# Optimization experiments

Hardware: AMD Instinct MI355X
Metric: run time of the kernel (lower is better)

Reference implementation:

```python
import jax, jax.numpy as jnp
import numpy as np

D_MODEL = 768
D_STATE = 16
D_CONV = 4
EXPAND = 2
HEADDIM = 64
D_INNER = EXPAND * D_MODEL          # 1536
NHEADS = D_INNER // HEADDIM         # 24
CONV_DIM = D_INNER + 2 * D_STATE    # 1568
D_IN_PROJ = 2 * D_INNER + 2 * D_STATE + NHEADS  # 3128
BATCH, SEQ = 4, 2048


def _mamba_params(key, scale=0.02):
    ks = jax.random.split(key, 5)
    return dict(
        in_w=jax.random.normal(ks[0], (D_MODEL, D_IN_PROJ), jnp.float32) * scale,
        conv_w=jax.random.normal(ks[1], (CONV_DIM, D_CONV), jnp.float32) * scale,
        conv_b=jnp.zeros((CONV_DIM,), jnp.float32),
        dt_bias=jax.random.normal(ks[2], (NHEADS,), jnp.float32) * 0.1,
        A_log=jnp.log(jax.random.uniform(ks[3], (NHEADS,), jnp.float32, 1.0, 16.0)),
        D=jnp.ones((NHEADS,), jnp.float32),
        norm_w=jnp.ones((D_INNER,), jnp.float32),
        out_w=jax.random.normal(ks[4], (D_INNER, D_MODEL), jnp.float32) * scale,
    )


def setup_inputs() -> dict:
    key = jax.random.key(0)
    kx, kf, kb, k1, k2 = jax.random.split(key, 5)
    f = _mamba_params(kf)
    b = _mamba_params(kb)
    k1a, k1b = jax.random.split(k1)
    inp = {
        'x': jax.random.normal(kx, (BATCH, SEQ, D_MODEL), jnp.float32),
        'ln1_w': jnp.ones((D_MODEL,), jnp.float32), 'ln1_b': jnp.zeros((D_MODEL,), jnp.float32),
        'ln2_w': jnp.ones((D_MODEL,), jnp.float32), 'ln2_b': jnp.zeros((D_MODEL,), jnp.float32),
        'ffn_w1': jax.random.normal(k1a, (2 * D_MODEL, 4 * D_MODEL), jnp.float32) * 0.02,
        'ffn_b1': jnp.zeros((4 * D_MODEL,), jnp.float32),
        'ffn_w2': jax.random.normal(k1b, (4 * D_MODEL, D_MODEL), jnp.float32) * 0.02,
        'ffn_b2': jnp.zeros((D_MODEL,), jnp.float32),
    }
    for name, p in (('f', f), ('b', b)):
        for k, v in p.items():
            inp[name + '_' + k] = v
    return inp


def _layernorm(x, w, b, eps=1e-5):
    m = jnp.mean(x, -1, keepdims=True)
    v = jnp.mean((x - m) ** 2, -1, keepdims=True)
    return (x - m) * jax.lax.rsqrt(v + eps) * w + b


def _mamba2(u, in_w, conv_w, conv_b, dt_bias, A_log, D, norm_w, out_w):
    b, l, _ = u.shape
    zxbcdt = u @ in_w                               # (b,l,d_in_proj)
    z = zxbcdt[..., :D_INNER]
    xBC = zxbcdt[..., D_INNER:D_INNER + CONV_DIM]
    dt = jax.nn.softplus(zxbcdt[..., -NHEADS:] + dt_bias)   # (b,l,h)
    # depthwise causal conv1d (kernel D_CONV) + SiLU
    xpad = jnp.pad(xBC, ((0, 0), (D_CONV - 1, 0), (0, 0)))
    xc = sum(conv_w[:, k] * xpad[:, k:k + l, :] for k in range(D_CONV)) + conv_b
    xc = jax.nn.silu(xc)
    xh = xc[..., :D_INNER].reshape(b, l, NHEADS, HEADDIM)
    Bm = xc[..., D_INNER:D_INNER + D_STATE]          # (b,l,n), ngroups=1
    Cm = xc[..., D_INNER + D_STATE:]                 # (b,l,n)
    A = -jnp.exp(A_log)                              # (h,)
    dA = jnp.exp(dt * A)                             # (b,l,h)

    def step(h, inp):
        dA_t, dt_t, B_t, C_t, x_t = inp              # (b,h),(b,h),(b,n),(b,n),(b,h,p)
        h = h * dA_t[:, :, None, None] + (dt_t[:, :, None] * x_t)[..., None] * B_t[:, None, None, :]
        y = jnp.einsum('bhpn,bn->bhp', h, C_t)
        return h, y

    h0 = jnp.zeros((b, NHEADS, HEADDIM, D_STATE), u.dtype)
    xs = (dA.transpose(1, 0, 2), dt.transpose(1, 0, 2), Bm.transpose(1, 0, 2),
          Cm.transpose(1, 0, 2), xh.transpose(1, 0, 2, 3))
    _, ys = jax.lax.scan(step, h0, xs)               # ys: (l,b,h,p)
    y = ys.transpose(1, 0, 2, 3) + D[None, None, :, None] * xh
    y = y.reshape(b, l, D_INNER)
    # gated RMSNorm: rmsnorm(y * silu(z)) * weight
    yz = y * jax.nn.silu(z)
    yz = yz * jax.lax.rsqrt(jnp.mean(yz * yz, -1, keepdims=True) + 1e-5) * norm_w
    return yz @ out_w


def reference(x, ln1_w, ln1_b, ln2_w, ln2_b,
              f_in_w, f_conv_w, f_conv_b, f_dt_bias, f_A_log, f_D, f_norm_w, f_out_w,
              b_in_w, b_conv_w, b_conv_b, b_dt_bias, b_A_log, b_D, b_norm_w, b_out_w,
              ffn_w1, ffn_b1, ffn_w2, ffn_b2):
    xn = _layernorm(x, ln1_w, ln1_b)
    fo = _mamba2(xn, f_in_w, f_conv_w, f_conv_b, f_dt_bias, f_A_log, f_D, f_norm_w, f_out_w)
    bo = _mamba2(jnp.flip(xn, 1), b_in_w, b_conv_w, b_conv_b, b_dt_bias, b_A_log, b_D, b_norm_w, b_out_w)
    bo = jnp.flip(bo, 1)
    bi = jnp.concatenate([fo, bo], -1)
    h = jax.nn.gelu(bi @ ffn_w1 + ffn_b1, approximate=False)
    h = jax.nn.gelu(h @ ffn_w2 + ffn_b2, approximate=False)
    # dropout is identity in eval mode
    return _layernorm(x + h, ln2_w, ln2_b)
```

## Files before the change

### kernel.cpp

```cpp
#include <hip/hip_runtime.h>
#include <math.h>

#define BATCH   4
#define SEQ     2048
#define DMODEL  768
#define DSTATE  16
#define DCONV   4
#define HEADDIM 64
#define DINNER  1536
#define NHEADS  24
#define CONVDIM 1568
#define DINPROJ 3128
#define DFFN    3072
#define ROWS    (BATCH*SEQ)
#define QCH     128
#define NCHUNK  (SEQ/QCH)

typedef __attribute__((ext_vector_type(8))) short bhalf8;
typedef __attribute__((ext_vector_type(4))) float floatx4;

__device__ __forceinline__ float gelu_f(float x) {
    return 0.5f * x * (1.0f + erff(x * 0.70710678118654752f));
}

__device__ __forceinline__ void splitRNE(float v, unsigned short& h, unsigned short& l) {
    unsigned u = __float_as_uint(v);
    unsigned rr = u + 0x7FFFu + ((u >> 16) & 1u);
    unsigned short hi = (unsigned short)(rr >> 16);
    float rem = v - __uint_as_float(((unsigned)hi) << 16);
    unsigned u2 = __float_as_uint(rem);
    unsigned r2 = u2 + 0x7FFFu + ((u2 >> 16) & 1u);
    h = hi;
    l = (unsigned short)(r2 >> 16);
}

__device__ __forceinline__ void gl16(const unsigned short* g, unsigned short* l) {
    __builtin_amdgcn_global_load_lds(
        (const __attribute__((address_space(1))) void*)g,
        (__attribute__((address_space(3))) void*)l, 16, 0, 0);
}

__device__ __forceinline__ float2 blockReduce2(float a, float b) {
    #pragma unroll
    for (int o = 32; o > 0; o >>= 1) {
        a += __shfl_down(a, o, 64);
        b += __shfl_down(b, o, 64);
    }
    __shared__ float sa[4], sb[4];
    int w = threadIdx.x >> 6, lane = threadIdx.x & 63;
    if (lane == 0) { sa[w] = a; sb[w] = b; }
    __syncthreads();
    if (threadIdx.x == 0) {
        int nw = blockDim.x >> 6;
        for (int i = 1; i < nw; ++i) { a += sa[i]; b += sb[i]; }
        sa[0] = a; sb[0] = b;
    }
    __syncthreads();
    return make_float2(sa[0], sb[0]);
}

__global__ __launch_bounds__(256) void ln_kernel(
    const float* __restrict__ x, const float* __restrict__ res,
    const float* __restrict__ w, const float* __restrict__ b,
    float* __restrict__ out)
{
    int r = blockIdx.x;
    const float* xr = x + (size_t)r * DMODEL;
    float v[3]; float s = 0.f, ss = 0.f;
    #pragma unroll
    for (int i = 0; i < 3; ++i) {
        int c = threadIdx.x + i * 256;
        float t = xr[c];
        if (res) t += res[(size_t)r * DMODEL + c];
        v[i] = t; s += t; ss += t * t;
    }
    float2 red = blockReduce2(s, ss);
    float mean = red.x * (1.0f / DMODEL);
    float var  = red.y * (1.0f / DMODEL) - mean * mean;
    float inv  = rsqrtf(var + 1e-5f);
    #pragma unroll
    for (int i = 0; i < 3; ++i) {
        int c = threadIdx.x + i * 256;
        out[(size_t)r * DMODEL + c] = (v[i] - mean) * inv * w[c] + b[c];
    }
}

__global__ __launch_bounds__(256) void ln_split_kernel(
    const float* __restrict__ x,
    const float* __restrict__ w, const float* __restrict__ b,
    unsigned short* __restrict__ H, unsigned short* __restrict__ L)
{
    int r = blockIdx.x;
    const float* xr = x + (size_t)r * DMODEL;
    float v[3]; float s = 0.f, ss = 0.f;
    #pragma unroll
    for (int i = 0; i < 3; ++i) {
        int c = threadIdx.x + i * 256;
        float t = xr[c];
        v[i] = t; s += t; ss += t * t;
    }
    float2 red = blockReduce2(s, ss);
    float mean = red.x * (1.0f / DMODEL);
    float var  = red.y * (1.0f / DMODEL) - mean * mean;
    float inv  = rsqrtf(var + 1e-5f);
    #pragma unroll
    for (int i = 0; i < 3; ++i) {
        int c = threadIdx.x + i * 256;
        float o = (v[i] - mean) * inv * w[c] + b[c];
        unsigned short h, l;
        splitRNE(o, h, l);
        H[(size_t)r * DMODEL + c] = h;
        L[(size_t)r * DMODEL + c] = l;
    }
}

__global__ __launch_bounds__(256) void wconv(
    const float* __restrict__ W, unsigned short* __restrict__ TH,
    unsigned short* __restrict__ TL, int K, int N)
{
    __shared__ float t[32][33];
    int tx = threadIdx.x & 31, ty = threadIdx.x >> 5;
    int kb = blockIdx.y * 32, nb = blockIdx.x * 32;
    #pragma unroll
    for (int i = 0; i < 4; ++i) {
        int k = kb + ty + i * 8, n = nb + tx;
        t[ty + i * 8][tx] = (k < K && n < N) ? W[(size_t)k * N + n] : 0.f;
    }
    __syncthreads();
    #pragma unroll
    for (int i = 0; i < 4; ++i) {
        int n = nb + ty + i * 8, k = kb + tx;
        if (n < N && k < K) {
            unsigned short hi, lo;
            splitRNE(t[tx][ty + i * 8], hi, lo);
            TH[(size_t)n * K + k] = hi;
            TL[(size_t)n * K + k] = lo;
        }
    }
}

__global__ __launch_bounds__(256) void gemm3(
    const unsigned short* __restrict__ AHg, const unsigned short* __restrict__ ALg,
    const unsigned short* __restrict__ BHg, const unsigned short* __restrict__ BLg,
    float* __restrict__ C, unsigned short* __restrict__ CHo, unsigned short* __restrict__ CLo,
    const float* __restrict__ bias,
    int M, int N, int K, int ldc, int coloff,
    int revA, int revC, int act)
{
    (void)M;
    __shared__ __align__(16) unsigned short AsH[128 * 32], AsL[128 * 32];
    __shared__ __align__(16) unsigned short BsH[128 * 32], BsL[128 * 32];

    const int tid = threadIdx.x;
    const int m0 = blockIdx.y * 128;
    const int n0 = blockIdx.x * 128;

    size_t aoff[2], boff[2];
    int lofs[2];
    #pragma unroll
    for (int q = 0; q < 2; ++q) {
        int row = (tid >> 2) + 64 * q;
        int sd  = (tid & 3) ^ ((row >> 1) & 3);
        int ar = m0 + row;
        if (revA) ar = (ar & ~(SEQ - 1)) + (SEQ - 1 - (ar & (SEQ - 1)));
        aoff[q] = (size_t)ar * K + sd * 8;
        boff[q] = (size_t)(n0 + row) * K + sd * 8;
        lofs[q] = (tid + 256 * q) * 8;
    }

    auto stage = [&](int k0) {
        #pragma unroll
        for (int q = 0; q < 2; ++q) {
            gl16(AHg + aoff[q] + k0, AsH + lofs[q]);
            gl16(ALg + aoff[q] + k0, AsL + lofs[q]);
            gl16(BHg + boff[q] + k0, BsH + lofs[q]);
            gl16(BLg + boff[q] + k0, BsL + lofs[q]);
        }
    };

    auto frag = [&](const unsigned short* buf, int row, int slot) -> bhalf8 {
        int sp = slot ^ ((row >> 1) & 3);
        return *(const bhalf8*)(buf + row * 32 + sp * 8);
    };

    const int w = tid >> 6, lane = tid & 63;
    const int rw = (w >> 1) * 64, cw = (w & 1) * 64;
    const int lr = lane & 15;
    const int lq = lane >> 4;

    floatx4 acc[4][4];
    const floatx4 fz = {0.f, 0.f, 0.f, 0.f};
    #pragma unroll
    for (int i = 0; i < 4; ++i)
        #pragma unroll
        for (int j = 0; j < 4; ++j) acc[i][j] = fz;

    const int ktiles = K >> 5;
    stage(0);
    for (int kt = 0; kt < ktiles; ++kt) {
        __syncthreads();
        bhalf8 ah[4], al[4], bh[4], bl[4];
        #pragma unroll
        for (int i = 0; i < 4; ++i) {
            int ra = rw + i * 16 + lr;
            int rb = cw + i * 16 + lr;
            ah[i] = frag(AsH, ra, lq);
            al[i] = frag(AsL, ra, lq);
            bh[i] = frag(BsH, rb, lq);
            bl[i] = frag(BsL, rb, lq);
        }
        __syncthreads();
        if (kt + 1 < ktiles) stage((kt + 1) * 32);
        #pragma unroll
        for (int i = 0; i < 4; ++i)
            #pragma unroll
            for (int j = 0; j < 4; ++j) {
                acc[i][j] = __builtin_amdgcn_mfma_f32_16x16x32_bf16(ah[i], bh[j], acc[i][j], 0, 0, 0);
                acc[i][j] = __builtin_amdgcn_mfma_f32_16x16x32_bf16(ah[i], bl[j], acc[i][j], 0, 0, 0);
                acc[i][j] = __builtin_amdgcn_mfma_f32_16x16x32_bf16(al[i], bh[j], acc[i][j], 0, 0, 0);
            }
    }

    #pragma unroll
    for (int i = 0; i < 4; ++i) {
        #pragma unroll
        for (int j = 0; j < 4; ++j) {
            int gc = n0 + cw + j * 16 + lr;
            if (gc < N) {
                float bv = bias ? bias[gc] : 0.f;
                #pragma unroll
                for (int rg = 0; rg < 4; ++rg) {
                    int gm = m0 + rw + i * 16 + lq * 4 + rg;
                    if (revC) gm = (gm & ~(SEQ - 1)) + (SEQ - 1 - (gm & (SEQ - 1)));
                    float v = acc[i][j][rg] + bv;
                    if (act) v = gelu_f(v);
                    size_t o = (size_t)gm * ldc + coloff + gc;
                    if (CHo) {
                        unsigned short h, l;
                        splitRNE(v, h, l);
                        CHo[o] = h; CLo[o] = l;
                    } else {
                        C[o] = v;
                    }
                }
            }
        }
    }
}

__global__ __launch_bounds__(64) void gemm1w(
    const unsigned short* __restrict__ AHg, const unsigned short* __restrict__ ALg,
    const unsigned short* __restrict__ BHg, const unsigned short* __restrict__ BLg,
    float* __restrict__ C, unsigned short* __restrict__ CHo, unsigned short* __restrict__ CLo,
    const float* __restrict__ bias,
    int M, int N, int K, int ldc, int coloff,
    int revA, int revC, int act)
{
    (void)M;
    __shared__ __align__(16) unsigned short AsH[64 * 32], AsL[64 * 32];
    __shared__ __align__(16) unsigned short BsH[64 * 32], BsL[64 * 32];

    const int tid = threadIdx.x;
    const int m0 = blockIdx.y * 64;
    const int n0 = blockIdx.x * 64;

    size_t aoff[4], boff[4];
    int lofs[4];
    #pragma unroll
    for (int q = 0; q < 4; ++q) {
        int row = (tid >> 2) + 16 * q;
        int sd  = (tid & 3) ^ ((row >> 1) & 3);
        int ar = m0 + row;
        if (revA) ar = (ar & ~(SEQ - 1)) + (SEQ - 1 - (ar & (SEQ - 1)));
        aoff[q] = (size_t)ar * K + sd * 8;
        boff[q] = (size_t)(n0 + row) * K + sd * 8;
        lofs[q] = (tid + 64 * q) * 8;
    }

    auto stage = [&](int k0) {
        #pragma unroll
        for (int q = 0; q < 4; ++q) {
            gl16(AHg + aoff[q] + k0, AsH + lofs[q]);
            gl16(ALg + aoff[q] + k0, AsL + lofs[q]);
            gl16(BHg + boff[q] + k0, BsH + lofs[q]);
            gl16(BLg + boff[q] + k0, BsL + lofs[q]);
        }
    };

    auto frag = [&](const unsigned short* buf, int row, int slot) -> bhalf8 {
        int sp = slot ^ ((row >> 1) & 3);
        return *(const bhalf8*)(buf + row * 32 + sp * 8);
    };

    const int lr = tid & 15;
    const int lq = tid >> 4;

    floatx4 acc[4][4];
    const floatx4 fz = {0.f, 0.f, 0.f, 0.f};
    #pragma unroll
    for (int i = 0; i < 4; ++i)
        #pragma unroll
        for (int j = 0; j < 4; ++j) acc[i][j] = fz;

    const int ktiles = K >> 5;
    stage(0);
    for (int kt = 0; kt < ktiles; ++kt) {
        asm volatile("s_waitcnt vmcnt(0)" ::: "memory");
        bhalf8 ah[4], al[4], bh[4], bl[4];
        #pragma unroll
        for (int i = 0; i < 4; ++i) {
            int rr = i * 16 + lr;
            ah[i] = frag(AsH, rr, lq);
            al[i] = frag(AsL, rr, lq);
            bh[i] = frag(BsH, rr, lq);
            bl[i] = frag(BsL, rr, lq);
        }
        asm volatile("s_waitcnt lgkmcnt(0)" ::: "memory");
        if (kt + 1 < ktiles) stage((kt + 1) * 32);
        #pragma unroll
        for (int i = 0; i < 4; ++i)
            #pragma unroll
            for (int j = 0; j < 4; ++j) {
                acc[i][j] = __builtin_amdgcn_mfma_f32_16x16x32_bf16(ah[i], bh[j], acc[i][j], 0, 0, 0);
                acc[i][j] = __builtin_amdgcn_mfma_f32_16x16x32_bf16(ah[i], bl[j], acc[i][j], 0, 0, 0);
                acc[i][j] = __builtin_amdgcn_mfma_f32_16x16x32_bf16(al[i], bh[j], acc[i][j], 0, 0, 0);
            }
    }

    #pragma unroll
    for (int i = 0; i < 4; ++i) {
        #pragma unroll
        for (int j = 0; j < 4; ++j) {
            int gc = n0 + j * 16 + lr;
            if (gc < N) {
                float bv = bias ? bias[gc] : 0.f;
                #pragma unroll
                for (int rg = 0; rg < 4; ++rg) {
                    int gm = m0 + i * 16 + lq * 4 + rg;
                    if (revC) gm = (gm & ~(SEQ - 1)) + (SEQ - 1 - (gm & (SEQ - 1)));
                    float v = acc[i][j][rg] + bv;
                    if (act) v = gelu_f(v);
                    size_t o = (size_t)gm * ldc + coloff + gc;
                    if (CHo) {
                        unsigned short h, l;
                        splitRNE(v, h, l);
                        CHo[o] = h; CLo[o] = l;
                    } else {
                        C[o] = v;
                    }
                }
            }
        }
    }
}

__global__ __launch_bounds__(256) void conv_kernel(
    const float* __restrict__ zx, const float* __restrict__ cw,
    const float* __restrict__ cb, float* __restrict__ xcv,
    float* __restrict__ bc,
    const float* __restrict__ dt_bias, const float* __restrict__ A_log,
    float* __restrict__ dtda)
{
    int cg = blockIdx.x * 256 + threadIdx.x;
    int r = blockIdx.y;
    if (cg < CONVDIM / 4) {
        int c = cg * 4;
        int t = r & (SEQ - 1);
        int rb = r & ~(SEQ - 1);
        float4 acc = *(const float4*)&cb[c];
        #pragma unroll
        for (int k = 0; k < DCONV; ++k) {
            int tt = t - (DCONV - 1) + k;
            if (tt >= 0) {
                float4 xv = *(const float4*)&zx[(size_t)(rb + tt) * DINPROJ + DINNER + c];
                acc.x += cw[(c + 0) * DCONV + k] * xv.x;
                acc.y += cw[(c + 1) * DCONV + k] * xv.y;
                acc.z += cw[(c + 2) * DCONV + k] * xv.z;
                acc.w += cw[(c + 3) * DCONV + k] * xv.w;
            }
        }
        float4 v;
        v.x = acc.x / (1.0f + expf(-acc.x));
        v.y = acc.y / (1.0f + expf(-acc.y));
        v.z = acc.z / (1.0f + expf(-acc.z));
        v.w = acc.w / (1.0f + expf(-acc.w));
        if (c < DINNER) *(float4*)&xcv[(size_t)r * DINNER + c] = v;
        else            *(float4*)&bc[(size_t)r * 32 + (c - DINNER)] = v;
    } else if (cg >= CONVDIM / 4 && cg < CONVDIM / 4 + NHEADS / 4) {
        int h0 = (cg - CONVDIM / 4) * 4;
        float4 zv = *(const float4*)&zx[(size_t)r * DINPROJ + (DINPROJ - NHEADS) + h0];
        float zz[4] = {zv.x, zv.y, zv.z, zv.w};
        #pragma unroll
        for (int j = 0; j < 4; ++j) {
            int h = h0 + j;
            float v = zz[j] + dt_bias[h];
            float dt = (v > 20.f) ? v : log1pf(expf(v));
            float A = -expf(A_log[h]);
            float2 o = make_float2(dt, expf(dt * A));
            *(float2*)&dtda[(size_t)r * 48 + 2 * h] = o;
        }
    }
}

__global__ __launch_bounds__(64) void scan_a(
    const float* __restrict__ xcv, const float* __restrict__ bc,
    const float* __restrict__ dtda, const float* __restrict__ Dp,
    float* __restrict__ yout, float* __restrict__ S, float* __restrict__ cd)
{
    int blk = blockIdx.x;
    int bh = blk / NCHUNK, c = blk - bh * NCHUNK;
    int b = bh / NHEADS, h = bh - b * NHEADS;
    int p = threadIdx.x;
    float hs[DSTATE] = {};
    float Dv = Dp[h];
    float cum = 1.f;
    int t0 = c * QCH;
    for (int t = t0; t < t0 + QCH; ++t) {
        size_t r = (size_t)b * SEQ + t;
        float2 dd = *(const float2*)&dtda[r * 48 + 2 * h];
        float dt = dd.x;
        float dA = dd.y;
        float x  = xcv[r * DINNER + h * HEADDIM + p];
        cum *= dA;
        float coef = dt * x;
        const float* bcr = bc + r * 32;
        float y = 0.f;
        #pragma unroll
        for (int n = 0; n < DSTATE; ++n) {
            hs[n] = hs[n] * dA + coef * bcr[n];
            y += hs[n] * bcr[16 + n];
        }
        yout[r * DINPROJ + DINNER + h * HEADDIM + p] = y + Dv * x;
        if (p == 0) cd[r * NHEADS + h] = cum;
    }
    float* Sp = S + (((size_t)bh * NCHUNK + c) * HEADDIM + p) * DSTATE;
    #pragma unroll
    for (int n = 0; n < DSTATE; ++n) Sp[n] = hs[n];
}

__global__ __launch_bounds__(64) void scan_b(
    const float* __restrict__ cd, float* __restrict__ S)
{
    int bh = blockIdx.x;
    int b = bh / NHEADS, h = bh - b * NHEADS;
    int p = threadIdx.x;
    float H[DSTATE] = {};
    for (int c = 0; c < NCHUNK; ++c) {
        float* Sp = S + (((size_t)bh * NCHUNK + c) * HEADDIM + p) * DSTATE;
        float P = cd[((size_t)b * SEQ + c * QCH + QCH - 1) * NHEADS + h];
        float s[DSTATE];
        #pragma unroll
        for (int n = 0; n < DSTATE; ++n) s[n] = Sp[n];
        #pragma unroll
        for (int n = 0; n < DSTATE; ++n) Sp[n] = H[n];
        #pragma unroll
        for (int n = 0; n < DSTATE; ++n) H[n] = P * H[n] + s[n];
    }
}

__global__ __launch_bounds__(64) void scan_c(
    const float* __restrict__ bc, const float* __restrict__ cd,
    const float* __restrict__ S, float* __restrict__ yout)
{
    int blk = blockIdx.x;
    int bh = blk / (NCHUNK - 1), c = blk - bh * (NCHUNK - 1) + 1;
    int b = bh / NHEADS, h = bh - b * NHEADS;
    int p = threadIdx.x;
    const float* Hp = S + (((size_t)bh * NCHUNK + c) * HEADDIM + p) * DSTATE;
    float H[DSTATE];
    #pragma unroll
    for (int n = 0; n < DSTATE; ++n) H[n] = Hp[n];
    int t0 = c * QCH;
    for (int t = t0; t < t0 + QCH; ++t) {
        size_t r = (size_t)b * SEQ + t;
        const float* Cr = bc + r * 32 + 16;
        float dot = 0.f;
        #pragma unroll
        for (int n = 0; n < DSTATE; ++n) dot += H[n] * Cr[n];
        float cum = cd[r * NHEADS + h];
        yout[r * DINPROJ + DINNER + h * HEADDIM + p] += cum * dot;
    }
}

__global__ __launch_bounds__(256) void gnorm_kernel(
    const float* __restrict__ zx, const float* __restrict__ nw,
    unsigned short* __restrict__ H, unsigned short* __restrict__ L)
{
    int r = blockIdx.x;
    const float* zr = zx + (size_t)r * DINPROJ;
    float v[6]; float ss = 0.f;
    #pragma unroll
    for (int i = 0; i < 6; ++i) {
        int c = threadIdx.x + i * 256;
        float z = zr[c];
        float y = zr[DINNER + c];
        float t = y * z / (1.0f + expf(-z));
        v[i] = t; ss += t * t;
    }
    float2 red = blockReduce2(ss, 0.f);
    float sc = rsqrtf(red.x * (1.0f / DINNER) + 1e-5f);
    #pragma unroll
    for (int i = 0; i < 6; ++i) {
        int c = threadIdx.x + i * 256;
        float o = v[i] * sc * nw[c];
        unsigned short h, l;
        splitRNE(o, h, l);
        H[(size_t)r * DINNER + c] = h;
        L[(size_t)r * DINNER + c] = l;
    }
}

extern "C" void kernel_launch(void* const* d_in, const int* in_sizes, int n_in,
                              void* d_out, int out_size, void* d_ws, size_t ws_size,
                              hipStream_t stream)
{
    (void)in_sizes; (void)n_in; (void)out_size; (void)ws_size;
    const float* x     = (const float*)d_in[0];
    const float* ln1w  = (const float*)d_in[1];
    const float* ln1b  = (const float*)d_in[2];
    const float* ln2w  = (const float*)d_in[3];
    const float* ln2b  = (const float*)d_in[4];
    const float* ffnw1 = (const float*)d_in[5];
    const float* ffnb1 = (const float*)d_in[6];
    const float* ffnw2 = (const float*)d_in[7];
    const float* ffnb2 = (const float*)d_in[8];
    const float* p[2][8];
    for (int d = 0; d < 2; ++d)
        for (int i = 0; i < 8; ++i)
            p[d][i] = (const float*)d_in[9 + d * 8 + i];

    float* ws   = (float*)d_ws;
    float* zx   = ws;
    float* bi   = zx + (size_t)ROWS * DINPROJ;
    float* S    = bi + (size_t)ROWS * DINNER;
    float* Wbuf = S  + (size_t)ROWS * DINNER;
    float* bcb  = Wbuf + 2402304;
    float* dtda = bcb + (size_t)ROWS * 32;
    float* Sbuf = Wbuf;
    float* cdbf = Wbuf + (size_t)BATCH * NHEADS * NCHUNK * HEADDIM * DSTATE;

    unsigned short* xnH = (unsigned short*)d_out;
    unsigned short* xnL = xnH + (size_t)ROWS * DMODEL;
    float* xcv = S;
    unsigned short* znH = (unsigned short*)S;
    unsigned short* znL = znH + (size_t)ROWS * DINNER;
    unsigned short* biH = (unsigned short*)bi;
    unsigned short* biL = biH + (size_t)ROWS * DINNER;
    unsigned short* hmH = (unsigned short*)zx;
    unsigned short* hmL = hmH + (size_t)ROWS * DFFN;
    float* ffo = S + 4718592;

    ln_split_kernel<<<ROWS, 256, 0, stream>>>(x, ln1w, ln1b, xnH, xnL);

    for (int d = 0; d < 2; ++d) {
        unsigned short* WH = (unsigned short*)Wbuf;
        unsigned short* WL = WH + (size_t)DINPROJ * DMODEL;
        wconv<<<dim3((DINPROJ + 31) / 32, DMODEL / 32), 256, 0, stream>>>(
            p[d][0], WH, WL, DMODEL, DINPROJ);
        gemm3<<<dim3((DINPROJ + 127) / 128, ROWS / 128), 256, 0, stream>>>(
            xnH, xnL, WH, WL, zx, nullptr, nullptr, nullptr,
            ROWS, DINPROJ, DMODEL, DINPROJ, 0, d, 0, 0);
        conv_kernel<<<dim3(2, ROWS), 256, 0, stream>>>(
            zx, p[d][1], p[d][2], xcv, bcb, p[d][3], p[d][4], dtda);
        scan_a<<<BATCH * NHEADS * NCHUNK, 64, 0, stream>>>(
            xcv, bcb, dtda, p[d][5], zx, Sbuf, cdbf);
        scan_b<<<BATCH * NHEADS, 64, 0, stream>>>(cdbf, Sbuf);
        scan_c<<<BATCH * NHEADS * (NCHUNK - 1), 64, 0, stream>>>(
            bcb, cdbf, Sbuf, zx);
        gnorm_kernel<<<ROWS, 256, 0, stream>>>(zx, p[d][6], znH, znL);
        unsigned short* WL2 = WH + (size_t)DMODEL * DINNER;
        wconv<<<dim3(DMODEL / 32, DINNER / 32), 256, 0, stream>>>(
            p[d][7], WH, WL2, DINNER, DMODEL);
        gemm1w<<<dim3(DMODEL / 64, ROWS / 64), 64, 0, stream>>>(
            znH, znL, WH, WL2, nullptr, biH, biL, nullptr,
            ROWS, DMODEL, DINNER, DINNER, d * DMODEL, 0, d, 0);
    }

    {
        unsigned short* WH = (unsigned short*)S;
        unsigned short* WL = WH + (size_t)DFFN * DINNER;
        wconv<<<dim3(DFFN / 32, DINNER / 32), 256, 0, stream>>>(
            ffnw1, WH, WL, DINNER, DFFN);
        gemm3<<<dim3(DFFN / 128, ROWS / 128), 256, 0, stream>>>(
            biH, biL, WH, WL, nullptr, hmH, hmL, ffnb1,
            ROWS, DFFN, DINNER, DFFN, 0, 0, 0, 1);
    }
    {
        unsigned short* WH = (unsigned short*)S;
        unsigned short* WL = WH + (size_t)DMODEL * DFFN;
        wconv<<<dim3(DMODEL / 32, DFFN / 32), 256, 0, stream>>>(
            ffnw2, WH, WL, DFFN, DMODEL);
        gemm1w<<<dim3(DMODEL / 64, ROWS / 64), 64, 0, stream>>>(
            hmH, hmL, WH, WL, ffo, nullptr, nullptr, ffnb2,
            ROWS, DMODEL, DFFN, DMODEL, 0, 0, 0, 1);
    }
    ln_kernel<<<ROWS, 256, 0, stream>>>(x, ffo, ln2w, ln2b, (float*)d_out);
}
```

Measured before the change: 1.712 ms.

## Batch both direction out-projections into one 128x128-tile GEMM launch

The per-direction out-projection GEMMs (64x64 tiles, one wave per block) are replaced by a single gemm3d launch. It covers both directions with 256-thread blocks, 128x128 tiles and four waves, picking the direction from blockIdx.y. The FFN2 GEMM also moves from gemm1w to the larger gemm3 kernel. Workspace buffers are reassigned so both gated-norm outputs and both converted weights stay live at the same time. The aims are better data reuse per block, fewer small launches and more parallel work per launch, at the cost of heavier buffer aliasing and block-level barriers in the k loop.

Result: faster. 1.538 ms (-10.2%).

```diff
diff --git a/kernel.cpp b/kernel.cpp
--- a/kernel.cpp
+++ b/kernel.cpp
@@ -248,38 +248,42 @@
     }
 }
 
-__global__ __launch_bounds__(64) void gemm1w(
-    const unsigned short* __restrict__ AHg, const unsigned short* __restrict__ ALg,
-    const unsigned short* __restrict__ BHg, const unsigned short* __restrict__ BLg,
-    float* __restrict__ C, unsigned short* __restrict__ CHo, unsigned short* __restrict__ CLo,
-    const float* __restrict__ bias,
-    int M, int N, int K, int ldc, int coloff,
-    int revA, int revC, int act)
-{
-    (void)M;
-    __shared__ __align__(16) unsigned short AsH[64 * 32], AsL[64 * 32];
-    __shared__ __align__(16) unsigned short BsH[64 * 32], BsL[64 * 32];
+__global__ __launch_bounds__(256) void gemm3d(
+    const unsigned short* __restrict__ A0H, const unsigned short* __restrict__ A0L,
+    const unsigned short* __restrict__ A1H, const unsigned short* __restrict__ A1L,
+    const unsigned short* __restrict__ W0H, const unsigned short* __restrict__ W0L,
+    const unsigned short* __restrict__ W1H, const unsigned short* __restrict__ W1L,
+    unsigned short* __restrict__ CHo, unsigned short* __restrict__ CLo)
+{
+    const int N = DMODEL, K = DINNER, ldc = DINNER;
+    const int dir = blockIdx.y >> 6;
+    const unsigned short* AHg = dir ? A1H : A0H;
+    const unsigned short* ALg = dir ? A1L : A0L;
+    const unsigned short* BHg = dir ? W1H : W0H;
+    const unsigned short* BLg = dir ? W1L : W0L;
+    const int coloff = dir * DMODEL;
+
+    __shared__ __align__(16) unsigned short AsH[128 * 32], AsL[128 * 32];
+    __shared__ __align__(16) unsigned short BsH[128 * 32], BsL[128 * 32];
 
     const int tid = threadIdx.x;
-    const int m0 = blockIdx.y * 64;
-    const int n0 = blockIdx.x * 64;
-
-    size_t aoff[4], boff[4];
-    int lofs[4];
-    #pragma unroll
-    for (int q = 0; q < 4; ++q) {
-        int row = (tid >> 2) + 16 * q;
+    const int m0 = (blockIdx.y & 63) * 128;
+    const int n0 = blockIdx.x * 128;
+
+    size_t aoff[2], boff[2];
+    int lofs[2];
+    #pragma unroll
+    for (int q = 0; q < 2; ++q) {
+        int row = (tid >> 2) + 64 * q;
         int sd  = (tid & 3) ^ ((row >> 1) & 3);
-        int ar = m0 + row;
-        if (revA) ar = (ar & ~(SEQ - 1)) + (SEQ - 1 - (ar & (SEQ - 1)));
-        aoff[q] = (size_t)ar * K + sd * 8;
+        aoff[q] = (size_t)(m0 + row) * K + sd * 8;
         boff[q] = (size_t)(n0 + row) * K + sd * 8;
-        lofs[q] = (tid + 64 * q) * 8;
+        lofs[q] = (tid + 256 * q) * 8;
     }
 
     auto stage = [&](int k0) {
         #pragma unroll
-        for (int q = 0; q < 4; ++q) {
+        for (int q = 0; q < 2; ++q) {
             gl16(AHg + aoff[q] + k0, AsH + lofs[q]);
             gl16(ALg + aoff[q] + k0, AsL + lofs[q]);
             gl16(BHg + boff[q] + k0, BsH + lofs[q]);
@@ -292,8 +296,10 @@
         return *(const bhalf8*)(buf + row * 32 + sp * 8);
     };
 
-    const int lr = tid & 15;
-    const int lq = tid >> 4;
+    const int w = tid >> 6, lane = tid & 63;
+    const int rw = (w >> 1) * 64, cw = (w & 1) * 64;
+    const int lr = lane & 15;
+    const int lq = lane >> 4;
 
     floatx4 acc[4][4];
     const floatx4 fz = {0.f, 0.f, 0.f, 0.f};
@@ -305,17 +311,18 @@
     const int ktiles = K >> 5;
     stage(0);
     for (int kt = 0; kt < ktiles; ++kt) {
-        asm volatile("s_waitcnt vmcnt(0)" ::: "memory");
+        __syncthreads();
         bhalf8 ah[4], al[4], bh[4], bl[4];
         #pragma unroll
         for (int i = 0; i < 4; ++i) {
-            int rr = i * 16 + lr;
-            ah[i] = frag(AsH, rr, lq);
-            al[i] = frag(AsL, rr, lq);
-            bh[i] = frag(BsH, rr, lq);
-            bl[i] = frag(BsL, rr, lq);
-        }
-        asm volatile("s_waitcnt lgkmcnt(0)" ::: "memory");
+            int ra = rw + i * 16 + lr;
+            int rb = cw + i * 16 + lr;
+            ah[i] = frag(AsH, ra, lq);
+            al[i] = frag(AsL, ra, lq);
+            bh[i] = frag(BsH, rb, lq);
+            bl[i] = frag(BsL, rb, lq);
+        }
+        __syncthreads();
         if (kt + 1 < ktiles) stage((kt + 1) * 32);
         #pragma unroll
         for (int i = 0; i < 4; ++i)
@@ -331,24 +338,16 @@
     for (int i = 0; i < 4; ++i) {
         #pragma unroll
         for (int j = 0; j < 4; ++j) {
-            int gc = n0 + j * 16 + lr;
-            if (gc < N) {
-                float bv = bias ? bias[gc] : 0.f;
-                #pragma unroll
-                for (int rg = 0; rg < 4; ++rg) {
-                    int gm = m0 + i * 16 + lq * 4 + rg;
-                    if (revC) gm = (gm & ~(SEQ - 1)) + (SEQ - 1 - (gm & (SEQ - 1)));
-                    float v = acc[i][j][rg] + bv;
-                    if (act) v = gelu_f(v);
-                    size_t o = (size_t)gm * ldc + coloff + gc;
-                    if (CHo) {
-                        unsigned short h, l;
-                        splitRNE(v, h, l);
-                        CHo[o] = h; CLo[o] = l;
-                    } else {
-                        C[o] = v;
-                    }
-                }
+            int gc = n0 + cw + j * 16 + lr;
+            #pragma unroll
+            for (int rg = 0; rg < 4; ++rg) {
+                int gm = m0 + rw + i * 16 + lq * 4 + rg;
+                if (dir) gm = (gm & ~(SEQ - 1)) + (SEQ - 1 - (gm & (SEQ - 1)));
+                float v = acc[i][j][rg];
+                size_t o = (size_t)gm * ldc + coloff + gc;
+                unsigned short h, l;
+                splitRNE(v, h, l);
+                CHo[o] = h; CLo[o] = l;
             }
         }
     }
@@ -542,12 +541,13 @@
     unsigned short* xnH = (unsigned short*)d_out;
     unsigned short* xnL = xnH + (size_t)ROWS * DMODEL;
     float* xcv = S;
-    unsigned short* znH = (unsigned short*)S;
-    unsigned short* znL = znH + (size_t)ROWS * DINNER;
-    unsigned short* biH = (unsigned short*)bi;
+    unsigned short* znH[2] = {(unsigned short*)bi, (unsigned short*)S};
+    unsigned short* znL[2] = {znH[0] + (size_t)ROWS * DINNER,
+                              znH[1] + (size_t)ROWS * DINNER};
+    unsigned short* biH = (unsigned short*)zx;
     unsigned short* biL = biH + (size_t)ROWS * DINNER;
-    unsigned short* hmH = (unsigned short*)zx;
-    unsigned short* hmL = hmH + (size_t)ROWS * DFFN;
+    unsigned short* hmH = (unsigned short*)(zx + (size_t)ROWS * DINNER);
+    unsigned short* hmL = (unsigned short*)bi;
     float* ffo = S + 4718592;
 
     ln_split_kernel<<<ROWS, 256, 0, stream>>>(x, ln1w, ln1b, xnH, xnL);
@@ -567,13 +567,21 @@
         scan_b<<<BATCH * NHEADS, 64, 0, stream>>>(cdbf, Sbuf);
         scan_c<<<BATCH * NHEADS * (NCHUNK - 1), 64, 0, stream>>>(
             bcb, cdbf, Sbuf, zx);
-        gnorm_kernel<<<ROWS, 256, 0, stream>>>(zx, p[d][6], znH, znL);
-        unsigned short* WL2 = WH + (size_t)DMODEL * DINNER;
+        gnorm_kernel<<<ROWS, 256, 0, stream>>>(zx, p[d][6], znH[d], znL[d]);
+    }
+
+    {
+        unsigned short* W0H = (unsigned short*)Wbuf;
+        unsigned short* W0L = W0H + (size_t)DMODEL * DINNER;
+        unsigned short* W1H = W0L + (size_t)DMODEL * DINNER;
+        unsigned short* W1L = W1H + (size_t)DMODEL * DINNER;
         wconv<<<dim3(DMODEL / 32, DINNER / 32), 256, 0, stream>>>(
-            p[d][7], WH, WL2, DINNER, DMODEL);
-        gemm1w<<<dim3(DMODEL / 64, ROWS / 64), 64, 0, stream>>>(
-            znH, znL, WH, WL2, nullptr, biH, biL, nullptr,
-            ROWS, DMODEL, DINNER, DINNER, d * DMODEL, 0, d, 0);
+            p[0][7], W0H, W0L, DINNER, DMODEL);
+        wconv<<<dim3(DMODEL / 32, DINNER / 32), 256, 0, stream>>>(
+            p[1][7], W1H, W1L, DINNER, DMODEL);
+        gemm3d<<<dim3(DMODEL / 128, 2 * ROWS / 128), 256, 0, stream>>>(
+            znH[0], znL[0], znH[1], znL[1],
+            W0H, W0L, W1H, W1L, biH, biL);
     }
 
     {
@@ -590,7 +598,7 @@
         unsigned short* WL = WH + (size_t)DMODEL * DFFN;
         wconv<<<dim3(DMODEL / 32, DFFN / 32), 256, 0, stream>>>(
             ffnw2, WH, WL, DFFN, DMODEL);
-        gemm1w<<<dim3(DMODEL / 64, ROWS / 64), 64, 0, stream>>>(
+        gemm3<<<dim3(DMODEL / 128, ROWS / 128), 256, 0, stream>>>(
             hmH, hmL, WH, WL, ffo, nullptr, nullptr, ffnb2,
             ROWS, DMODEL, DFFN, DMODEL, 0, 0, 0, 1);
     }
```
